# Kernel optimization log

Hardware: AMD Instinct MI355X
Metric: run time of the kernel (lower is better)

The kernel has to match this reference:

```python
import jax, jax.numpy as jnp
import numpy as np

N, E = 50000, 800000
IN_DIM, OUT_DIM, REL_DIM = 128, 64, 32
NEG_SLOPE = 0.01  # torch F.leaky_relu default


def setup_inputs() -> dict:
    key = jax.random.key(0)
    ks = jax.random.split(key, 12)
    return {
        "h": jax.random.normal(ks[0], (N, IN_DIM), jnp.float32),
        "relation": jax.random.normal(ks[1], (E, REL_DIM), jnp.float32),
        "score": jax.random.normal(ks[2], (E, 1), jnp.float32),
        "timestamp": jax.random.normal(ks[3], (E, 1), jnp.float32),
        "src": jax.random.randint(ks[4], (E,), 0, N, jnp.int32),
        "dst": jax.random.randint(ks[5], (E,), 0, N, jnp.int32),
        "W_n": jax.random.normal(ks[6], (IN_DIM, OUT_DIM), jnp.float32) / np.sqrt(IN_DIM),
        "W_r": jax.random.normal(ks[7], (REL_DIM, OUT_DIM), jnp.float32) / np.sqrt(REL_DIM),
        "W_s": jax.random.normal(ks[8], (1, OUT_DIM), jnp.float32),
        "W_t": jax.random.normal(ks[9], (1, OUT_DIM), jnp.float32),
        "a": jax.random.normal(ks[10], (5 * OUT_DIM,), jnp.float32) / np.sqrt(5 * OUT_DIM),
    }


def reference(h, relation, score, timestamp, src, dst, W_n, W_r, W_s, W_t, a):
    D = W_n.shape[1]
    z = h @ W_n                     # (N, D)
    er = relation @ W_r             # (E, D)
    es = score @ W_s                # (E, D)
    et = timestamp @ W_t            # (E, D)
    z_src = z[src]                  # (E, D) gather
    z_dst = z[dst]                  # (E, D) gather
    # attn_fc on concat([z_src, z_dst, er, es, et]) == sum of slice dot-products
    a1, a2, a3, a4, a5 = (a[0:D], a[D:2*D], a[2*D:3*D], a[3*D:4*D], a[4*D:5*D])
    logit = z_src @ a1 + z_dst @ a2 + er @ a3 + es @ a4 + et @ a5  # (E,)
    logit = jnp.where(logit >= 0, logit, NEG_SLOPE * logit)        # leaky_relu
    # segment softmax over edges grouped by dst node
    n = z.shape[0]
    seg_max = jax.ops.segment_max(logit, dst, num_segments=n)     # (N,)
    ex = jnp.exp(logit - seg_max[dst])                             # (E,)
    seg_sum = jax.ops.segment_sum(ex, dst, num_segments=n)        # (N,)
    alpha = ex / seg_sum[dst]                                      # (E,)
    # weighted scatter-sum of source features to dst nodes
    h_out = jax.ops.segment_sum(alpha[:, None] * z_src, dst, num_segments=n)  # (N, D)
    return h_out
```

## Files before the change

kernel.cpp:

```cpp
#include <hip/hip_runtime.h>
#include <hip/hip_fp16.h>

#define IN_DIM 128
#define OUT_DIM 64
#define REL_DIM 32
#define NEG_SLOPE 0.01f

typedef float    vfloat4 __attribute__((ext_vector_type(4)));
typedef unsigned vuint4  __attribute__((ext_vector_type(4)));
typedef unsigned vuint2  __attribute__((ext_vector_type(2)));

__device__ __forceinline__ unsigned pack_edge(int s, float lg) {
    return ((unsigned)s << 16) | (unsigned)__half_as_ushort(__float2half(lg));
}
__device__ __forceinline__ int unpack_src(unsigned u) { return (int)(u >> 16); }
__device__ __forceinline__ float unpack_lg(unsigned u) {
    return __half2float(__ushort_as_half((unsigned short)(u & 0xffffu)));
}

__global__ __launch_bounds__(256) void k_node(const float* __restrict__ h,
                                              const float* __restrict__ W_n,
                                              const float* __restrict__ a,
                                              __half* __restrict__ zh,
                                              float* __restrict__ s1,
                                              float* __restrict__ s2,
                                              int* __restrict__ deg, int n) {
    __shared__ float hs[IN_DIM * 65];
    __shared__ float s1p[4][64], s2p[4][64];
    int base = blockIdx.x * 64;

    for (int i = threadIdx.x; i < 64 * 32; i += 256) {
        int r = i >> 5;
        int c4 = i & 31;
        float4 v = make_float4(0.f, 0.f, 0.f, 0.f);
        if (base + r < n) v = ((const float4*)(h + (size_t)(base + r) * IN_DIM))[c4];
        int k0 = c4 * 4;
        hs[(k0 + 0) * 65 + r] = v.x;
        hs[(k0 + 1) * 65 + r] = v.y;
        hs[(k0 + 2) * 65 + r] = v.z;
        hs[(k0 + 3) * 65 + r] = v.w;
    }
    __syncthreads();

    int lane = threadIdx.x & 63;
    int w = __builtin_amdgcn_readfirstlane(threadIdx.x >> 6);
    int c0 = w * 16;
    int row = base + lane;

    float acc[16];
    #pragma unroll
    for (int j = 0; j < 16; ++j) acc[j] = 0.f;

    const float* __restrict__ Wslice = W_n + c0;
    #pragma unroll 4
    for (int k = 0; k < IN_DIM; ++k) {
        float hv = hs[k * 65 + lane];
        const float* __restrict__ Wr = Wslice + k * OUT_DIM;
        #pragma unroll
        for (int j = 0; j < 16; ++j) acc[j] = fmaf(hv, Wr[j], acc[j]);
    }

    float p1 = 0.f, p2 = 0.f;
    #pragma unroll
    for (int j = 0; j < 16; ++j) {
        p1 = fmaf(acc[j], a[c0 + j], p1);
        p2 = fmaf(acc[j], a[OUT_DIM + c0 + j], p2);
    }
    s1p[w][lane] = p1;
    s2p[w][lane] = p2;

    if (row < n) {
        union { __half2 hp[8]; vuint4 v[2]; } uz;
        #pragma unroll
        for (int j = 0; j < 8; ++j)
            uz.hp[j] = __floats2half2_rn(acc[2 * j], acc[2 * j + 1]);
        vuint4* zp = (vuint4*)(zh + (size_t)row * OUT_DIM + c0);
        zp[0] = uz.v[0];
        zp[1] = uz.v[1];
    }
    __syncthreads();
    if (threadIdx.x < 64 && base + (int)threadIdx.x < n) {
        int l = threadIdx.x;
        s1[base + l] = s1p[0][l] + s1p[1][l] + s1p[2][l] + s1p[3][l];
        s2[base + l] = s2p[0][l] + s2p[1][l] + s2p[2][l] + s2p[3][l];
        deg[base + l] = 0;
    }
}

__global__ __launch_bounds__(256) void k_edge(const float* __restrict__ rel,
                                              const float* __restrict__ score,
                                              const float* __restrict__ ts,
                                              const int* __restrict__ src,
                                              const int* __restrict__ dst,
                                              const float* __restrict__ s1,
                                              const float* __restrict__ s2,
                                              const float* __restrict__ W_r,
                                              const float* __restrict__ W_s,
                                              const float* __restrict__ W_t,
                                              const float* __restrict__ a,
                                              unsigned* __restrict__ payload,
                                              int* __restrict__ deg, int E) {
    __shared__ float wra3[REL_DIM];
    __shared__ float c45[2];
    int t = threadIdx.x;
    if (t < REL_DIM) {
        const float* a3 = a + 2 * OUT_DIM;
        float acc = 0.f;
        for (int d = 0; d < OUT_DIM; ++d) acc += W_r[t * OUT_DIM + d] * a3[d];
        wra3[t] = acc;
    } else if (t == 32 || t == 33) {
        const float* Wx = (t == 32) ? W_s : W_t;
        const float* ax = a + (t == 32 ? 3 : 4) * OUT_DIM;
        float acc = 0.f;
        for (int d = 0; d < OUT_DIM; ++d) acc += Wx[d] * ax[d];
        c45[t - 32] = acc;
    }
    __syncthreads();
    int e = blockIdx.x * blockDim.x + threadIdx.x;
    if (e >= E) return;
    float c4 = c45[0], c5 = c45[1];
    const vfloat4* r4 = (const vfloat4*)(rel + (size_t)e * REL_DIM);
    float acc = 0.f;
    #pragma unroll
    for (int j = 0; j < REL_DIM / 4; ++j) {
        vfloat4 v = __builtin_nontemporal_load(r4 + j);
        acc += v.x * wra3[4 * j] + v.y * wra3[4 * j + 1] +
               v.z * wra3[4 * j + 2] + v.w * wra3[4 * j + 3];
    }
    int s = __builtin_nontemporal_load(src + e);
    int d = __builtin_nontemporal_load(dst + e);
    float sc = __builtin_nontemporal_load(score + e);
    float tv = __builtin_nontemporal_load(ts + e);
    float lg = s1[s] + s2[d] + acc + sc * c4 + tv * c5;
    lg = (lg >= 0.f) ? lg : NEG_SLOPE * lg;
    __builtin_nontemporal_store(pack_edge(s, lg), payload + e);
    atomicAdd(deg + d, 1);
}

__global__ __launch_bounds__(256) void k_scan1(const int* __restrict__ deg,
                                               int* __restrict__ incl,
                                               int* __restrict__ partial, int n) {
    __shared__ int tmp[256];
    int i = blockIdx.x * 256 + threadIdx.x;
    int v = (i < n) ? deg[i] : 0;
    tmp[threadIdx.x] = v;
    __syncthreads();
    #pragma unroll
    for (int o = 1; o < 256; o <<= 1) {
        int t = (threadIdx.x >= o) ? tmp[threadIdx.x - o] : 0;
        __syncthreads();
        tmp[threadIdx.x] += t;
        __syncthreads();
    }
    if (i < n) incl[i] = tmp[threadIdx.x];
    if (threadIdx.x == 255) partial[blockIdx.x] = tmp[255];
}

__global__ __launch_bounds__(256) void k_scan2(int* __restrict__ partial, int nb) {
    __shared__ int tmp[256];
    int v = (threadIdx.x < nb) ? partial[threadIdx.x] : 0;
    tmp[threadIdx.x] = v;
    __syncthreads();
    #pragma unroll
    for (int o = 1; o < 256; o <<= 1) {
        int t = (threadIdx.x >= o) ? tmp[threadIdx.x - o] : 0;
        __syncthreads();
        tmp[threadIdx.x] += t;
        __syncthreads();
    }
    if (threadIdx.x < nb) partial[threadIdx.x] = tmp[threadIdx.x] - v;
}

__global__ __launch_bounds__(256) void k_scan3(const int* __restrict__ deg,
                                               const int* __restrict__ incl,
                                               const int* __restrict__ partial,
                                               int* __restrict__ off,
                                               int* __restrict__ cnt, int n, int E) {
    int i = blockIdx.x * 256 + threadIdx.x;
    if (i < n) {
        int o = incl[i] - deg[i] + partial[i >> 8];
        off[i] = o;
        cnt[i] = o;
    }
    if (i == 0) off[n] = E;
}

__global__ __launch_bounds__(256) void k_fill(const unsigned* __restrict__ payload,
                                              const int* __restrict__ dst,
                                              int* __restrict__ cnt,
                                              unsigned* __restrict__ pedge, int E) {
    int e = blockIdx.x * blockDim.x + threadIdx.x;
    if (e >= E) return;
    unsigned p = __builtin_nontemporal_load(payload + e);
    int d = __builtin_nontemporal_load(dst + e);
    int pos = atomicAdd(cnt + d, 1);
    pedge[pos] = p;
}

__global__ __launch_bounds__(256) void k_out(const int* __restrict__ off,
                                             const unsigned* __restrict__ pedge,
                                             const __half* __restrict__ zh,
                                             float* __restrict__ out, int n) {
    int lane = threadIdx.x & 63;
    int wave = (blockIdx.x * blockDim.x + threadIdx.x) >> 6;
    int nwaves = (gridDim.x * blockDim.x) >> 6;
    int eg = lane >> 4;
    int dl = lane & 15;
    for (int node = wave; node < n; node += nwaves) {
        int start = off[node], end = off[node + 1];
        int deg = end - start;
        float4 acc = make_float4(0.f, 0.f, 0.f, 0.f);
        if (deg > 0 && deg <= 64) {
            unsigned pe = 0xfc00u;
            if (lane < deg) pe = pedge[start + lane];
            float v = unpack_lg(pe);
            float m = v;
            #pragma unroll
            for (int o = 32; o > 0; o >>= 1) m = fmaxf(m, __shfl_xor(m, o, 64));
            float ex = __expf(v - m);
            float ssum = ex;
            #pragma unroll
            for (int o = 32; o > 0; o >>= 1) ssum += __shfl_xor(ssum, o, 64);
            float alpha = ex * (1.0f / ssum);
            int   srcl  = unpack_src(pe);
            for (int j0 = 0; j0 < deg; j0 += 4) {
                int j = j0 + eg;
                int jc = (j < 64) ? j : 63;
                float wj = __shfl(alpha, jc, 64);
                int  sj = __shfl(srcl, jc, 64);
                if (j < deg) {
                    vuint2 u = *(const vuint2*)(zh + (size_t)sj * OUT_DIM + dl * 4);
                    union { unsigned u; __half2 h; } ca, cb;
                    ca.u = u.x; cb.u = u.y;
                    float2 f01 = __half22float2(ca.h);
                    float2 f23 = __half22float2(cb.h);
                    acc.x = fmaf(wj, f01.x, acc.x);
                    acc.y = fmaf(wj, f01.y, acc.y);
                    acc.z = fmaf(wj, f23.x, acc.z);
                    acc.w = fmaf(wj, f23.y, acc.w);
                }
            }
        } else if (deg > 64) {
            float m = -3.4e38f;
            for (int j = start + lane; j < end; j += 64)
                m = fmaxf(m, unpack_lg(pedge[j]));
            #pragma unroll
            for (int o = 32; o > 0; o >>= 1) m = fmaxf(m, __shfl_xor(m, o, 64));
            float ssum = 0.f;
            for (int j = start + lane; j < end; j += 64)
                ssum += __expf(unpack_lg(pedge[j]) - m);
            #pragma unroll
            for (int o = 32; o > 0; o >>= 1) ssum += __shfl_xor(ssum, o, 64);
            float inv = 1.0f / ssum;
            for (int j0 = start; j0 < end; j0 += 4) {
                int j = j0 + eg;
                if (j < end) {
                    unsigned pe = pedge[j];
                    float wj = __expf(unpack_lg(pe) - m) * inv;
                    vuint2 u = *(const vuint2*)(zh + (size_t)unpack_src(pe) * OUT_DIM + dl * 4);
                    union { unsigned u; __half2 h; } ca, cb;
                    ca.u = u.x; cb.u = u.y;
                    float2 f01 = __half22float2(ca.h);
                    float2 f23 = __half22float2(cb.h);
                    acc.x = fmaf(wj, f01.x, acc.x);
                    acc.y = fmaf(wj, f01.y, acc.y);
                    acc.z = fmaf(wj, f23.x, acc.z);
                    acc.w = fmaf(wj, f23.y, acc.w);
                }
            }
        }
        #pragma unroll
        for (int o = 16; o <= 32; o <<= 1) {
            acc.x += __shfl_xor(acc.x, o, 64);
            acc.y += __shfl_xor(acc.y, o, 64);
            acc.z += __shfl_xor(acc.z, o, 64);
            acc.w += __shfl_xor(acc.w, o, 64);
        }
        if (eg == 0) ((float4*)(out + (size_t)node * OUT_DIM))[dl] = acc;
    }
}

extern "C" void kernel_launch(void* const* d_in, const int* in_sizes, int n_in,
                              void* d_out, int out_size, void* d_ws, size_t ws_size,
                              hipStream_t stream) {
    const float* h         = (const float*)d_in[0];
    const float* relation  = (const float*)d_in[1];
    const float* score     = (const float*)d_in[2];
    const float* timestamp = (const float*)d_in[3];
    const int*   src       = (const int*)d_in[4];
    const int*   dst       = (const int*)d_in[5];
    const float* W_n       = (const float*)d_in[6];
    const float* W_r       = (const float*)d_in[7];
    const float* W_s       = (const float*)d_in[8];
    const float* W_t       = (const float*)d_in[9];
    const float* a         = (const float*)d_in[10];

    int n = in_sizes[0] / IN_DIM;
    int E = in_sizes[4];
    int nb1 = (n + 255) / 256;
    int nbE = (E + 255) / 256;

    __half*   zh      = (__half*)d_ws;
    float*    s1      = (float*)(zh + (size_t)n * OUT_DIM);
    float*    s2      = s1 + n;
    unsigned* payload = (unsigned*)(s2 + n);
    unsigned* pedge   = payload + E;
    int*      deg     = (int*)(pedge + E);
    int*      incl    = deg + n;
    int*      off     = incl + n;
    int*      cnt     = off + n + 1;
    int*      partial = cnt + n;

    float* out = (float*)d_out;

    k_node<<<(n + 63) / 64, 256, 0, stream>>>(h, W_n, a, zh, s1, s2, deg, n);
    k_edge<<<nbE, 256, 0, stream>>>(relation, score, timestamp, src, dst,
                                    s1, s2, W_r, W_s, W_t, a, payload, deg, E);
    k_scan1<<<nb1, 256, 0, stream>>>(deg, incl, partial, n);
    k_scan2<<<1, 256, 0, stream>>>(partial, nb1);
    k_scan3<<<nb1, 256, 0, stream>>>(deg, incl, partial, off, cnt, n, E);
    k_fill<<<nbE, 256, 0, stream>>>(payload, dst, cnt, pedge, E);
    k_out<<<(n + 3) / 4, 256, 0, stream>>>(off, pedge, zh, out, n);
}
```

Before: 332.3 us.

## Count degrees first, fuse edge logit compute with CSR fill, defer node terms

Adds a lightweight degree-count kernel that reads only dst, so the edge-feature kernel can run after the scan and write packed edges straight into CSR slots, removing the intermediate payload buffer and the separate fill pass. The per-node s1/s2 terms and leaky-relu move into the output kernel, so the packed half now holds only the edge-only logit part. The edge kernel processes two edges per thread. In exchange, the output kernel does extra random s1 gathers, and fp16 now holds a partial logit, which changes rounding behaviour. The zh stores are also split into narrower 8-byte writes.

```diff
diff --git a/kernel.cpp b/kernel.cpp
--- a/kernel.cpp
+++ b/kernel.cpp
@@ -7,14 +7,14 @@
 #define NEG_SLOPE 0.01f
 
 typedef float    vfloat4 __attribute__((ext_vector_type(4)));
-typedef unsigned vuint4  __attribute__((ext_vector_type(4)));
 typedef unsigned vuint2  __attribute__((ext_vector_type(2)));
-
-__device__ __forceinline__ unsigned pack_edge(int s, float lg) {
-    return ((unsigned)s << 16) | (unsigned)__half_as_ushort(__float2half(lg));
+typedef int      vint4   __attribute__((ext_vector_type(4)));
+
+__device__ __forceinline__ unsigned pack_edge(int s, float ce) {
+    return ((unsigned)s << 16) | (unsigned)__half_as_ushort(__float2half(ce));
 }
 __device__ __forceinline__ int unpack_src(unsigned u) { return (int)(u >> 16); }
-__device__ __forceinline__ float unpack_lg(unsigned u) {
+__device__ __forceinline__ float unpack_ce(unsigned u) {
     return __half2float(__ushort_as_half((unsigned short)(u & 0xffffu)));
 }
 
@@ -70,13 +70,15 @@
     s2p[w][lane] = p2;
 
     if (row < n) {
-        union { __half2 hp[8]; vuint4 v[2]; } uz;
+        union { __half2 hp[8]; vuint2 v[4]; } uz;
         #pragma unroll
         for (int j = 0; j < 8; ++j)
             uz.hp[j] = __floats2half2_rn(acc[2 * j], acc[2 * j + 1]);
-        vuint4* zp = (vuint4*)(zh + (size_t)row * OUT_DIM + c0);
+        vuint2* zp = (vuint2*)(zh + (size_t)row * OUT_DIM + c0);
         zp[0] = uz.v[0];
         zp[1] = uz.v[1];
+        zp[2] = uz.v[2];
+        zp[3] = uz.v[3];
     }
     __syncthreads();
     if (threadIdx.x < 64 && base + (int)threadIdx.x < n) {
@@ -87,19 +89,106 @@
     }
 }
 
+__global__ __launch_bounds__(256) void k_count(const int* __restrict__ dst,
+                                               int* __restrict__ deg, int E) {
+    int i0 = (blockIdx.x * blockDim.x + threadIdx.x) * 4;
+    if (i0 + 3 < E) {
+        vint4 dd = __builtin_nontemporal_load((const vint4*)(dst + i0));
+        atomicAdd(deg + dd.x, 1);
+        atomicAdd(deg + dd.y, 1);
+        atomicAdd(deg + dd.z, 1);
+        atomicAdd(deg + dd.w, 1);
+    } else {
+        for (int j = i0; j < E; ++j) atomicAdd(deg + dst[j], 1);
+    }
+}
+
+__global__ __launch_bounds__(256) void k_scan1(const int* __restrict__ deg,
+                                               int* __restrict__ incl,
+                                               int* __restrict__ partial, int n) {
+    __shared__ int tmp[256];
+    int i = blockIdx.x * 256 + threadIdx.x;
+    int v = (i < n) ? deg[i] : 0;
+    tmp[threadIdx.x] = v;
+    __syncthreads();
+    #pragma unroll
+    for (int o = 1; o < 256; o <<= 1) {
+        int t = (threadIdx.x >= o) ? tmp[threadIdx.x - o] : 0;
+        __syncthreads();
+        tmp[threadIdx.x] += t;
+        __syncthreads();
+    }
+    if (i < n) incl[i] = tmp[threadIdx.x];
+    if (threadIdx.x == 255) partial[blockIdx.x] = tmp[255];
+}
+
+__global__ __launch_bounds__(256) void k_scan2(int* __restrict__ partial, int nb) {
+    __shared__ int tmp[256];
+    int v = (threadIdx.x < nb) ? partial[threadIdx.x] : 0;
+    tmp[threadIdx.x] = v;
+    __syncthreads();
+    #pragma unroll
+    for (int o = 1; o < 256; o <<= 1) {
+        int t = (threadIdx.x >= o) ? tmp[threadIdx.x - o] : 0;
+        __syncthreads();
+        tmp[threadIdx.x] += t;
+        __syncthreads();
+    }
+    if (threadIdx.x < nb) partial[threadIdx.x] = tmp[threadIdx.x] - v;
+}
+
+__global__ __launch_bounds__(256) void k_scan3(const int* __restrict__ deg,
+                                               const int* __restrict__ incl,
+                                               const int* __restrict__ partial,
+                                               int* __restrict__ off,
+                                               int* __restrict__ cnt, int n, int E) {
+    int i = blockIdx.x * 256 + threadIdx.x;
+    if (i < n) {
+        int o = incl[i] - deg[i] + partial[i >> 8];
+        off[i] = o;
+        cnt[i] = o;
+    }
+    if (i == 0) off[n] = E;
+}
+
+__device__ __forceinline__ void edge_body(int e,
+                                          const float* __restrict__ rel,
+                                          const float* __restrict__ score,
+                                          const float* __restrict__ ts,
+                                          const int* __restrict__ src,
+                                          const int* __restrict__ dst,
+                                          const float* wra3, float c4, float c5,
+                                          int* __restrict__ cnt,
+                                          unsigned* __restrict__ pedge) {
+    const vfloat4* r4 = (const vfloat4*)(rel + (size_t)e * REL_DIM);
+    float acc = 0.f;
+    #pragma unroll
+    for (int j = 0; j < REL_DIM / 4; ++j) {
+        vfloat4 v = __builtin_nontemporal_load(r4 + j);
+        acc += v.x * wra3[4 * j] + v.y * wra3[4 * j + 1] +
+               v.z * wra3[4 * j + 2] + v.w * wra3[4 * j + 3];
+    }
+    int s = __builtin_nontemporal_load(src + e);
+    int d = __builtin_nontemporal_load(dst + e);
+    float sc = __builtin_nontemporal_load(score + e);
+    float tv = __builtin_nontemporal_load(ts + e);
+    float ce = acc + sc * c4 + tv * c5;
+    int pos = atomicAdd(cnt + d, 1);
+    pedge[pos] = pack_edge(s, ce);
+}
+
 __global__ __launch_bounds__(256) void k_edge(const float* __restrict__ rel,
                                               const float* __restrict__ score,
                                               const float* __restrict__ ts,
                                               const int* __restrict__ src,
                                               const int* __restrict__ dst,
-                                              const float* __restrict__ s1,
-                                              const float* __restrict__ s2,
                                               const float* __restrict__ W_r,
                                               const float* __restrict__ W_s,
                                               const float* __restrict__ W_t,
                                               const float* __restrict__ a,
-                                              unsigned* __restrict__ payload,
-                                              int* __restrict__ deg, int E) {
+                                              int* __restrict__ cnt,
+                                              unsigned* __restrict__ pedge,
+                                              int E, int G) {
     __shared__ float wra3[REL_DIM];
     __shared__ float c45[2];
     int t = threadIdx.x;
@@ -116,89 +205,19 @@
         c45[t - 32] = acc;
     }
     __syncthreads();
-    int e = blockIdx.x * blockDim.x + threadIdx.x;
-    if (e >= E) return;
     float c4 = c45[0], c5 = c45[1];
-    const vfloat4* r4 = (const vfloat4*)(rel + (size_t)e * REL_DIM);
-    float acc = 0.f;
-    #pragma unroll
-    for (int j = 0; j < REL_DIM / 4; ++j) {
-        vfloat4 v = __builtin_nontemporal_load(r4 + j);
-        acc += v.x * wra3[4 * j] + v.y * wra3[4 * j + 1] +
-               v.z * wra3[4 * j + 2] + v.w * wra3[4 * j + 3];
-    }
-    int s = __builtin_nontemporal_load(src + e);
-    int d = __builtin_nontemporal_load(dst + e);
-    float sc = __builtin_nontemporal_load(score + e);
-    float tv = __builtin_nontemporal_load(ts + e);
-    float lg = s1[s] + s2[d] + acc + sc * c4 + tv * c5;
-    lg = (lg >= 0.f) ? lg : NEG_SLOPE * lg;
-    __builtin_nontemporal_store(pack_edge(s, lg), payload + e);
-    atomicAdd(deg + d, 1);
-}
-
-__global__ __launch_bounds__(256) void k_scan1(const int* __restrict__ deg,
-                                               int* __restrict__ incl,
-                                               int* __restrict__ partial, int n) {
-    __shared__ int tmp[256];
-    int i = blockIdx.x * 256 + threadIdx.x;
-    int v = (i < n) ? deg[i] : 0;
-    tmp[threadIdx.x] = v;
-    __syncthreads();
-    #pragma unroll
-    for (int o = 1; o < 256; o <<= 1) {
-        int t = (threadIdx.x >= o) ? tmp[threadIdx.x - o] : 0;
-        __syncthreads();
-        tmp[threadIdx.x] += t;
-        __syncthreads();
-    }
-    if (i < n) incl[i] = tmp[threadIdx.x];
-    if (threadIdx.x == 255) partial[blockIdx.x] = tmp[255];
-}
-
-__global__ __launch_bounds__(256) void k_scan2(int* __restrict__ partial, int nb) {
-    __shared__ int tmp[256];
-    int v = (threadIdx.x < nb) ? partial[threadIdx.x] : 0;
-    tmp[threadIdx.x] = v;
-    __syncthreads();
-    #pragma unroll
-    for (int o = 1; o < 256; o <<= 1) {
-        int t = (threadIdx.x >= o) ? tmp[threadIdx.x - o] : 0;
-        __syncthreads();
-        tmp[threadIdx.x] += t;
-        __syncthreads();
-    }
-    if (threadIdx.x < nb) partial[threadIdx.x] = tmp[threadIdx.x] - v;
-}
-
-__global__ __launch_bounds__(256) void k_scan3(const int* __restrict__ deg,
-                                               const int* __restrict__ incl,
-                                               const int* __restrict__ partial,
-                                               int* __restrict__ off,
-                                               int* __restrict__ cnt, int n, int E) {
-    int i = blockIdx.x * 256 + threadIdx.x;
-    if (i < n) {
-        int o = incl[i] - deg[i] + partial[i >> 8];
-        off[i] = o;
-        cnt[i] = o;
-    }
-    if (i == 0) off[n] = E;
-}
-
-__global__ __launch_bounds__(256) void k_fill(const unsigned* __restrict__ payload,
-                                              const int* __restrict__ dst,
-                                              int* __restrict__ cnt,
-                                              unsigned* __restrict__ pedge, int E) {
-    int e = blockIdx.x * blockDim.x + threadIdx.x;
-    if (e >= E) return;
-    unsigned p = __builtin_nontemporal_load(payload + e);
-    int d = __builtin_nontemporal_load(dst + e);
-    int pos = atomicAdd(cnt + d, 1);
-    pedge[pos] = p;
+    int tid = blockIdx.x * blockDim.x + threadIdx.x;
+    if (tid < G)
+        edge_body(tid, rel, score, ts, src, dst, wra3, c4, c5, cnt, pedge);
+    int e2 = tid + G;
+    if (e2 < E)
+        edge_body(e2, rel, score, ts, src, dst, wra3, c4, c5, cnt, pedge);
 }
 
 __global__ __launch_bounds__(256) void k_out(const int* __restrict__ off,
                                              const unsigned* __restrict__ pedge,
+                                             const float* __restrict__ s1,
+                                             const float* __restrict__ s2,
                                              const __half* __restrict__ zh,
                                              float* __restrict__ out, int n) {
     int lane = threadIdx.x & 63;
@@ -211,13 +230,18 @@
         int deg = end - start;
         float4 acc = make_float4(0.f, 0.f, 0.f, 0.f);
         if (deg > 0 && deg <= 64) {
-            unsigned pe = 0xfc00u;
-            if (lane < deg) pe = pedge[start + lane];
-            float v = unpack_lg(pe);
-            float m = v;
+            float s2n = s2[node];
+            unsigned pe = 0;
+            float lg = -3.4e38f;
+            if (lane < deg) {
+                pe = pedge[start + lane];
+                float raw = s1[unpack_src(pe)] + s2n + unpack_ce(pe);
+                lg = (raw >= 0.f) ? raw : NEG_SLOPE * raw;
+            }
+            float m = lg;
             #pragma unroll
             for (int o = 32; o > 0; o >>= 1) m = fmaxf(m, __shfl_xor(m, o, 64));
-            float ex = __expf(v - m);
+            float ex = (lane < deg) ? __expf(lg - m) : 0.f;
             float ssum = ex;
             #pragma unroll
             for (int o = 32; o > 0; o >>= 1) ssum += __shfl_xor(ssum, o, 64);
@@ -241,14 +265,23 @@
                 }
             }
         } else if (deg > 64) {
+            float s2n = s2[node];
             float m = -3.4e38f;
-            for (int j = start + lane; j < end; j += 64)
-                m = fmaxf(m, unpack_lg(pedge[j]));
+            for (int j = start + lane; j < end; j += 64) {
+                unsigned pe = pedge[j];
+                float raw = s1[unpack_src(pe)] + s2n + unpack_ce(pe);
+                float lg = (raw >= 0.f) ? raw : NEG_SLOPE * raw;
+                m = fmaxf(m, lg);
+            }
             #pragma unroll
             for (int o = 32; o > 0; o >>= 1) m = fmaxf(m, __shfl_xor(m, o, 64));
             float ssum = 0.f;
-            for (int j = start + lane; j < end; j += 64)
-                ssum += __expf(unpack_lg(pedge[j]) - m);
+            for (int j = start + lane; j < end; j += 64) {
+                unsigned pe = pedge[j];
+                float raw = s1[unpack_src(pe)] + s2n + unpack_ce(pe);
+                float lg = (raw >= 0.f) ? raw : NEG_SLOPE * raw;
+                ssum += __expf(lg - m);
+            }
             #pragma unroll
             for (int o = 32; o > 0; o >>= 1) ssum += __shfl_xor(ssum, o, 64);
             float inv = 1.0f / ssum;
@@ -256,7 +289,9 @@
                 int j = j0 + eg;
                 if (j < end) {
                     unsigned pe = pedge[j];
-                    float wj = __expf(unpack_lg(pe) - m) * inv;
+                    float raw = s1[unpack_src(pe)] + s2n + unpack_ce(pe);
+                    float lg = (raw >= 0.f) ? raw : NEG_SLOPE * raw;
+                    float wj = __expf(lg - m) * inv;
                     vuint2 u = *(const vuint2*)(zh + (size_t)unpack_src(pe) * OUT_DIM + dl * 4);
                     union { unsigned u; __half2 h; } ca, cb;
                     ca.u = u.x; cb.u = u.y;
@@ -298,13 +333,12 @@
     int n = in_sizes[0] / IN_DIM;
     int E = in_sizes[4];
     int nb1 = (n + 255) / 256;
-    int nbE = (E + 255) / 256;
+    int G = (E + 1) / 2;
 
     __half*   zh      = (__half*)d_ws;
     float*    s1      = (float*)(zh + (size_t)n * OUT_DIM);
     float*    s2      = s1 + n;
-    unsigned* payload = (unsigned*)(s2 + n);
-    unsigned* pedge   = payload + E;
+    unsigned* pedge   = (unsigned*)(s2 + n);
     int*      deg     = (int*)(pedge + E);
     int*      incl    = deg + n;
     int*      off     = incl + n;
@@ -314,11 +348,11 @@
     float* out = (float*)d_out;
 
     k_node<<<(n + 63) / 64, 256, 0, stream>>>(h, W_n, a, zh, s1, s2, deg, n);
-    k_edge<<<nbE, 256, 0, stream>>>(relation, score, timestamp, src, dst,
-                                    s1, s2, W_r, W_s, W_t, a, payload, deg, E);
+    k_count<<<(E + 1023) / 1024, 256, 0, stream>>>(dst, deg, E);
     k_scan1<<<nb1, 256, 0, stream>>>(deg, incl, partial, n);
     k_scan2<<<1, 256, 0, stream>>>(partial, nb1);
     k_scan3<<<nb1, 256, 0, stream>>>(deg, incl, partial, off, cnt, n, E);
-    k_fill<<<nbE, 256, 0, stream>>>(payload, dst, cnt, pedge, E);
-    k_out<<<(n + 3) / 4, 256, 0, stream>>>(off, pedge, zh, out, n);
-}
+    k_edge<<<(G + 255) / 256, 256, 0, stream>>>(relation, score, timestamp, src, dst,
+                                                W_r, W_s, W_t, a, cnt, pedge, E, G);
+    k_out<<<(n + 3) / 4, 256, 0, stream>>>(off, pedge, s1, s2, zh, out, n);
+}
```

Result: no change. 335.4 us (+0.9%).
